# Kernel optimization log

Hardware: AMD Instinct MI355X
Metric: run time of the kernel (lower is better)

Reference implementation:

```python
import jax, jax.numpy as jnp
import numpy as np

N = 50000        # num nodes
E = 800000       # num edges
F_IN = 128
H1 = 256
H2 = 256
C = 64


def _sage_conv(x, edge_index, W_l, b_l, W_r):
    """PyG SAGEConv (mean aggr): lin_l(mean over in-neighbors of x_j) + lin_r(x)."""
    src = edge_index[0]
    dst = edge_index[1]
    n = x.shape[0]
    # gather messages [E, d] then segment-mean into [N, d]
    agg = jax.ops.segment_sum(x[src], dst, num_segments=n)
    cnt = jax.ops.segment_sum(jnp.ones((edge_index.shape[1],), x.dtype), dst, num_segments=n)
    mean = agg / jnp.maximum(cnt, 1.0)[:, None]
    return mean @ W_l + b_l + x @ W_r


def setup_inputs() -> dict:
    key = jax.random.key(0)
    ks = jax.random.split(key, 10)
    x = jax.random.normal(ks[0], (N, F_IN), dtype=jnp.float32)
    edge_index = jax.random.randint(ks[1], (2, E), 0, N, dtype=jnp.int64)
    s1 = 1.0 / np.sqrt(F_IN)
    s2 = 1.0 / np.sqrt(H1)
    s3 = 1.0 / np.sqrt(H2)
    return {
        "x": x,
        "edge_index": edge_index,
        "W1_l": jax.random.uniform(ks[2], (F_IN, H1), jnp.float32, -s1, s1),
        "b1": jnp.zeros((H1,), jnp.float32),
        "W1_r": jax.random.uniform(ks[3], (F_IN, H1), jnp.float32, -s1, s1),
        "W2_l": jax.random.uniform(ks[4], (H1, H2), jnp.float32, -s2, s2),
        "b2": jnp.zeros((H2,), jnp.float32),
        "W2_r": jax.random.uniform(ks[5], (H1, H2), jnp.float32, -s2, s2),
        "Wc": jax.random.uniform(ks[6], (H2, C), jnp.float32, -s3, s3),
        "bc": jax.random.uniform(ks[7], (C,), jnp.float32, -s3, s3),
    }


def reference(x, edge_index, W1_l, b1, W1_r, W2_l, b2, W2_r, Wc, bc):
    # inference mode: dropout is identity
    h = jax.nn.relu(_sage_conv(x, edge_index, W1_l, b1, W1_r))
    h = jax.nn.relu(_sage_conv(h, edge_index, W2_l, b2, W2_r))
    return h @ Wc + bc
```

## Files before the change

kernel.cpp:

```cpp
#include <hip/hip_runtime.h>
#include <hip/hip_bf16.h>


#define F_IN 128
#define H1_DIM 256
#define H2_DIM 256
#define C_DIM 64

typedef __attribute__((ext_vector_type(8))) _Float16 f16x8;
typedef __attribute__((ext_vector_type(8))) unsigned short u16x8;
typedef __attribute__((ext_vector_type(4))) float f32x4;

__device__ __forceinline__ unsigned short f2h(float f) {
    return __builtin_bit_cast(unsigned short, (_Float16)f);
}
__device__ __forceinline__ float h2f(unsigned short h) {
    return (float)__builtin_bit_cast(_Float16, h);
}

__global__ void k_detect(const unsigned int* __restrict__ ei, int* __restrict__ flag) {
    if (blockIdx.x == 0 && threadIdx.x == 0) {
        int is64 = 1;
        for (int i = 1; i < 256; i += 2) {
            if (ei[i] != 0u) { is64 = 0; break; }
        }
        *flag = is64;
    }
}

__device__ __forceinline__ int ei_at(const void* ei, const int* flag, long long idx) {
    return (*flag) ? (int)((const long long*)ei)[idx] : ((const int*)ei)[idx];
}

__global__ void k_degree(const void* __restrict__ ei, const int* __restrict__ flag,
                         int* __restrict__ cnt, int E) {
    int i = blockIdx.x * blockDim.x + threadIdx.x;
    if (i >= E) return;
    atomicAdd(&cnt[ei_at(ei, flag, (long long)E + i)], 1);
}

__global__ void k_scan1(const int* __restrict__ cnt, int* __restrict__ rowptr,
                        int* __restrict__ bsum, int n) {
    __shared__ int s[256];
    int i = blockIdx.x * 256 + threadIdx.x;
    int v = (i < n) ? cnt[i] : 0;
    s[threadIdx.x] = v;
    __syncthreads();
    for (int off = 1; off < 256; off <<= 1) {
        int t = (threadIdx.x >= off) ? s[threadIdx.x - off] : 0;
        __syncthreads();
        s[threadIdx.x] += t;
        __syncthreads();
    }
    if (i < n) rowptr[i] = s[threadIdx.x] - v;
    if (threadIdx.x == 255) bsum[blockIdx.x] = s[255];
}

__global__ void k_scan2(const int* __restrict__ bsum, int* __restrict__ boff, int nb) {
    __shared__ int s[1024];
    int t = threadIdx.x;
    int v = (t < nb) ? bsum[t] : 0;
    s[t] = v;
    __syncthreads();
    for (int off = 1; off < 1024; off <<= 1) {
        int u = (t >= off) ? s[t - off] : 0;
        __syncthreads();
        s[t] += u;
        __syncthreads();
    }
    if (t < nb) boff[t] = s[t] - v;
}

__global__ void k_scan3(int* __restrict__ rowptr, const int* __restrict__ boff,
                        int n, int total) {
    int i = blockIdx.x * 256 + threadIdx.x;
    if (i < n) rowptr[i] += boff[i >> 8];
    if (i == 0) rowptr[n] = total;
}

__global__ void k_scatter(const void* __restrict__ ei, const int* __restrict__ flag,
                          const int* __restrict__ rowptr, int* __restrict__ pos,
                          int* __restrict__ col, int E) {
    int i = blockIdx.x * blockDim.x + threadIdx.x;
    if (i >= E) return;
    int s = ei_at(ei, flag, i);
    int d = ei_at(ei, flag, (long long)E + i);
    int p = atomicAdd(&pos[d], 1);
    col[rowptr[d] + p] = s;
}

__global__ void k_prep_x(const float* __restrict__ x, unsigned short* __restrict__ xh,
                         int n4) {
    int i = blockIdx.x * 256 + threadIdx.x;
    if (i >= n4) return;
    float4 v = ((const float4*)x)[i];
    ushort4 h;
    h.x = f2h(v.x);
    h.y = f2h(v.y);
    h.z = f2h(v.z);
    h.w = f2h(v.w);
    ((ushort4*)xh)[i] = h;
}

struct WPrep {
    const float* W;
    unsigned short* wT;
    int K;
    int NN;
};

__global__ void k_prep_w(WPrep w0, WPrep w1, WPrep w2, WPrep w3, WPrep w4) {
    WPrep wp;
    switch (blockIdx.y) {
        case 0: wp = w0; break;
        case 1: wp = w1; break;
        case 2: wp = w2; break;
        case 3: wp = w3; break;
        default: wp = w4; break;
    }
    int total = wp.K * wp.NN;
    for (int i = blockIdx.x * 256 + threadIdx.x; i < total; i += gridDim.x * 256) {
        int k = i / wp.NN, n = i % wp.NN;
        wp.wT[(size_t)n * wp.K + k] = f2h(wp.W[i]);
    }
}

__global__ void k_agg1(const unsigned short* __restrict__ xh,
                       const int* __restrict__ rowptr, const int* __restrict__ col,
                       unsigned short* __restrict__ mean, int n) {
    int w = blockIdx.x * 4 + (threadIdx.x >> 6);
    int lane = threadIdx.x & 63;
    if (w >= n) return;
    int q = lane >> 4;
    int ch = (lane & 15) * 8;
    int beg = rowptr[w], end = rowptr[w + 1];
    float inv = 1.0f / fmaxf((float)(end - beg), 1.0f);

    float a[8];
#pragma unroll
    for (int c = 0; c < 8; ++c) a[c] = 0.f;

    int j = beg + q;
    for (; j + 4 < end; j += 8) {
        int c0 = col[j], c1 = col[j + 4];
        u16x8 r0 = *(const u16x8*)(xh + (size_t)c0 * 128 + ch);
        u16x8 r1 = *(const u16x8*)(xh + (size_t)c1 * 128 + ch);
#pragma unroll
        for (int c = 0; c < 8; ++c) a[c] += h2f(r0[c]) + h2f(r1[c]);
    }
    if (j < end) {
        u16x8 r0 = *(const u16x8*)(xh + (size_t)col[j] * 128 + ch);
#pragma unroll
        for (int c = 0; c < 8; ++c) a[c] += h2f(r0[c]);
    }

#pragma unroll
    for (int c = 0; c < 8; ++c) a[c] += __shfl_xor(a[c], 16);
#pragma unroll
    for (int c = 0; c < 8; ++c) a[c] += __shfl_xor(a[c], 32);

    if (q == 0) {
        u16x8 o;
#pragma unroll
        for (int c = 0; c < 8; ++c) o[c] = f2h(a[c] * inv);
        *(u16x8*)(mean + (size_t)w * 128 + ch) = o;
    }
}

__global__ void k_agg2(const unsigned short* __restrict__ hh,
                       const int* __restrict__ rowptr, const int* __restrict__ col,
                       unsigned short* __restrict__ mean, int n) {
    int w = blockIdx.x * 4 + (threadIdx.x >> 6);
    int lane = threadIdx.x & 63;
    if (w >= n) return;
    int h = lane >> 5;
    int ch = (lane & 31) * 8;
    int beg = rowptr[w], end = rowptr[w + 1];
    float inv = 1.0f / fmaxf((float)(end - beg), 1.0f);

    float a[8];
#pragma unroll
    for (int c = 0; c < 8; ++c) a[c] = 0.f;

    int j = beg + h;
    for (; j + 2 < end; j += 4) {
        int c0 = col[j], c1 = col[j + 2];
        u16x8 r0 = *(const u16x8*)(hh + (size_t)c0 * 256 + ch);
        u16x8 r1 = *(const u16x8*)(hh + (size_t)c1 * 256 + ch);
#pragma unroll
        for (int c = 0; c < 8; ++c) a[c] += h2f(r0[c]) + h2f(r1[c]);
    }
    if (j < end) {
        u16x8 r0 = *(const u16x8*)(hh + (size_t)col[j] * 256 + ch);
#pragma unroll
        for (int c = 0; c < 8; ++c) a[c] += h2f(r0[c]);
    }

#pragma unroll
    for (int c = 0; c < 8; ++c) a[c] += __shfl_xor(a[c], 32);

    if (h == 0) {
        u16x8 o;
#pragma unroll
        for (int c = 0; c < 8; ++c) o[c] = f2h(a[c] * inv);
        *(u16x8*)(mean + (size_t)w * 256 + ch) = o;
    }
}

struct Loads {
    const unsigned short* a[2];
    const unsigned short* b[2];
};

template <int BN, int NLOAD, int KS, bool RELU, int OUTMODE>
__global__ __launch_bounds__(256, 4) void k_mfma_gemm(
    Loads L, const float* __restrict__ bias,
    float* __restrict__ Cf, unsigned short* __restrict__ Ch, int M, int NN) {
    constexpr int BM = 128;
    constexpr int WAVES = 4;
    constexpr int WCN = 2;
    constexpr int WM = 64;
    constexpr int WN = BN / WCN;
    constexpr int FM = 4;
    constexpr int FN = WN / 16;
    constexpr int ACH = 16;
    constexpr int BCH = BN / 8;

    __shared__ unsigned short sA[BM * 64];
    __shared__ unsigned short sB[BN * 64];

    const int tid = threadIdx.x;
    const int lane = tid & 63;
    const int wid = tid >> 6;
    const int wr = wid / WCN, wc = wid % WCN;

    const int nbn = NN / BN;
    const int bm = (nbn == 1) ? blockIdx.x : blockIdx.x / nbn;
    const int bn = (nbn == 1) ? 0 : blockIdx.x % nbn;
    const int row0 = bm * BM;
    const int col0 = bn * BN;

    f32x4 acc[FM][FN];
#pragma unroll
    for (int m = 0; m < FM; ++m)
#pragma unroll
        for (int n = 0; n < FN; ++n) acc[m][n] = (f32x4){0.f, 0.f, 0.f, 0.f};

    const int l7 = lane & 7;
    const int l15 = lane & 15;
    const int q = lane >> 4;
    const int st_r = lane >> 3;
    const int st_k = 8 * (l7 ^ st_r);

    for (int ld = 0; ld < NLOAD; ++ld) {
        const unsigned short* Ag = L.a[ld];
        const unsigned short* Bg = L.b[ld];

        for (int k0 = 0; k0 < KS; k0 += 64) {
#pragma unroll
            for (int c = wid; c < ACH; c += WAVES) {
                int gr = row0 + c * 8 + st_r;
                if (gr >= M) gr = 0;
                const unsigned short* gp = Ag + (size_t)gr * KS + k0 + st_k;
                __builtin_amdgcn_global_load_lds(
                    (const __attribute__((address_space(1))) unsigned int*)gp,
                    (__attribute__((address_space(3))) unsigned int*)(sA + c * 512),
                    16, 0, 0);
            }
#pragma unroll
            for (int c = wid; c < BCH; c += WAVES) {
                int gn = col0 + c * 8 + st_r;
                const unsigned short* gp = Bg + (size_t)gn * KS + k0 + st_k;
                __builtin_amdgcn_global_load_lds(
                    (const __attribute__((address_space(1))) unsigned int*)gp,
                    (__attribute__((address_space(3))) unsigned int*)(sB + c * 512),
                    16, 0, 0);
            }
            __syncthreads();

#pragma unroll
            for (int ks = 0; ks < 2; ++ks) {
                const int sidx = 8 * ((q + 4 * ks) ^ l7);
                f16x8 af[FM], bf[FN];
#pragma unroll
                for (int m = 0; m < FM; ++m) {
                    int rb = wr * WM + m * 16 + l15;
                    af[m] = *(const f16x8*)(sA + (size_t)rb * 64 + sidx);
                }
#pragma unroll
                for (int n = 0; n < FN; ++n) {
                    int cb = wc * WN + n * 16 + l15;
                    bf[n] = *(const f16x8*)(sB + (size_t)cb * 64 + sidx);
                }
#pragma unroll
                for (int m = 0; m < FM; ++m)
#pragma unroll
                    for (int n = 0; n < FN; ++n)
                        acc[m][n] = __builtin_amdgcn_mfma_f32_16x16x32_f16(
                            af[m], bf[n], acc[m][n], 0, 0, 0);
            }
            __syncthreads();
        }
    }

#pragma unroll
    for (int m = 0; m < FM; ++m) {
#pragma unroll
        for (int n = 0; n < FN; ++n) {
            int col = col0 + wc * WN + n * 16 + l15;
            float bb = bias[col];
#pragma unroll
            for (int r = 0; r < 4; ++r) {
                int row = row0 + wr * WM + m * 16 + q * 4 + r;
                if (row < M) {
                    float t = acc[m][n][r] + bb;
                    if (RELU) t = fmaxf(t, 0.f);
                    if (OUTMODE == 0) {
                        Cf[(size_t)row * NN + col] = t;
                    } else {
                        Ch[(size_t)row * NN + col] = f2h(t);
                    }
                }
            }
        }
    }
}

extern "C" void kernel_launch(void* const* d_in, const int* in_sizes, int n_in,
                              void* d_out, int out_size, void* d_ws, size_t ws_size,
                              hipStream_t stream) {
    const float* x   = (const float*)d_in[0];
    const void*  ei  = d_in[1];
    const float* W1l = (const float*)d_in[2];
    const float* b1  = (const float*)d_in[3];
    const float* W1r = (const float*)d_in[4];
    const float* W2l = (const float*)d_in[5];
    const float* b2  = (const float*)d_in[6];
    const float* W2r = (const float*)d_in[7];
    const float* Wc  = (const float*)d_in[8];
    const float* bc  = (const float*)d_in[9];
    float* out = (float*)d_out;

    const int N = in_sizes[0] / F_IN;
    const int E = in_sizes[1] / 2;

    typedef unsigned short u16;

    char* w = (char*)d_ws;
    size_t off = 0;
    auto carve = [&](size_t bytes) -> char* {
        char* p = w + off;
        off = (off + bytes + 255) & ~(size_t)255;
        return p;
    };
    int* cnt    = (int*)carve((size_t)N * 4);
    int* pos    = (int*)carve((size_t)N * 4);
    int* rowptr = (int*)carve((size_t)(N + 1) * 4);
    int* bsum   = (int*)carve(1024 * 4);
    int* boff   = (int*)carve(1024 * 4);
    int* flag   = (int*)carve(256);
    int* col    = (int*)carve((size_t)E * 4);

    u16* xh     = (u16*)carve((size_t)N * F_IN * 2);
    u16* agg    = (u16*)carve((size_t)N * 256 * 2);
    u16* h1     = (u16*)carve((size_t)N * 256 * 2);
    u16* h2     = (u16*)carve((size_t)N * 256 * 2);

    u16* w1lT   = (u16*)carve((size_t)F_IN * H1_DIM * 2);
    u16* w1rT   = (u16*)carve((size_t)F_IN * H1_DIM * 2);
    u16* w2lT   = (u16*)carve((size_t)H1_DIM * H2_DIM * 2);
    u16* w2rT   = (u16*)carve((size_t)H1_DIM * H2_DIM * 2);
    u16* wcT    = (u16*)carve((size_t)H2_DIM * C_DIM * 2);
    (void)ws_size;

    hipMemsetAsync(cnt, 0, (char*)rowptr - (char*)cnt, stream);

    k_detect<<<1, 64, 0, stream>>>((const unsigned int*)ei, flag);
    k_degree<<<(E + 255) / 256, 256, 0, stream>>>(ei, flag, cnt, E);
    int nb = (N + 255) / 256;
    k_scan1<<<nb, 256, 0, stream>>>(cnt, rowptr, bsum, N);
    k_scan2<<<1, 1024, 0, stream>>>(bsum, boff, nb);
    k_scan3<<<nb, 256, 0, stream>>>(rowptr, boff, N, E);
    k_scatter<<<(E + 255) / 256, 256, 0, stream>>>(ei, flag, rowptr, pos, col, E);

    k_prep_x<<<((N * F_IN / 4) + 255) / 256, 256, 0, stream>>>(x, xh, N * F_IN / 4);
    {
        WPrep w0{W1l, w1lT, F_IN, H1_DIM};
        WPrep w1{W1r, w1rT, F_IN, H1_DIM};
        WPrep w2{W2l, w2lT, H1_DIM, H2_DIM};
        WPrep w3{W2r, w2rT, H1_DIM, H2_DIM};
        WPrep w4{Wc, wcT, H2_DIM, C_DIM};
        dim3 g(64, 5);
        k_prep_w<<<g, 256, 0, stream>>>(w0, w1, w2, w3, w4);
    }

    const int nbm = (N + 127) / 128;

    k_agg1<<<(N + 3) / 4, 256, 0, stream>>>(xh, rowptr, col, agg, N);
    {
        Loads L;
        L.a[0] = agg; L.b[0] = w1lT;
        L.a[1] = xh;  L.b[1] = w1rT;
        k_mfma_gemm<128, 2, 128, true, 1><<<nbm * (H1_DIM / 128), 256, 0, stream>>>(
            L, b1, nullptr, h1, N, H1_DIM);
    }

    k_agg2<<<(N + 3) / 4, 256, 0, stream>>>(h1, rowptr, col, agg, N);
    {
        Loads L;
        L.a[0] = agg; L.b[0] = w2lT;
        L.a[1] = h1;  L.b[1] = w2rT;
        k_mfma_gemm<128, 2, 256, true, 1><<<nbm * (H2_DIM / 128), 256, 0, stream>>>(
            L, b2, nullptr, h2, N, H2_DIM);
    }

    {
        Loads L;
        L.a[0] = h2; L.b[0] = wcT;
        L.a[1] = nullptr; L.b[1] = nullptr;
        k_mfma_gemm<64, 1, 256, false, 0><<<nbm, 256, 0, stream>>>(
            L, bc, out, nullptr, N, C_DIM);
    }
}
```

Before: 334.8 us.

## Gather neighbor features from column-sliced tables to shrink aggregation working set

Node features and layer-1 outputs are also written in a column-sliced layout (32-channel slices stored contiguously per slice). A new templated aggregation kernel gives each block one slice, and four lanes cover one node's 64-byte slice row. The aim is to keep each gather pass's working set small enough to stay in cache across random neighbor accesses. The cost is extra writes of duplicate tables in the prep and GEMM epilogue, plus scattered 2-byte stores in the GEMM epilogue.

```diff
diff --git a/kernel.cpp b/kernel.cpp
--- a/kernel.cpp
+++ b/kernel.cpp
@@ -90,7 +90,7 @@
 }
 
 __global__ void k_prep_x(const float* __restrict__ x, unsigned short* __restrict__ xh,
-                         int n4) {
+                         unsigned short* __restrict__ xs, int n4, int N) {
     int i = blockIdx.x * 256 + threadIdx.x;
     if (i >= n4) return;
     float4 v = ((const float4*)x)[i];
@@ -100,6 +100,10 @@
     h.z = f2h(v.z);
     h.w = f2h(v.w);
     ((ushort4*)xh)[i] = h;
+    int row = i >> 5;
+    int c0 = (i & 31) * 4;
+    int s = c0 >> 5;
+    *(ushort4*)(xs + ((size_t)s * N + row) * 32 + (c0 & 31)) = h;
 }
 
 struct WPrep {
@@ -125,86 +129,42 @@
     }
 }
 
-__global__ void k_agg1(const unsigned short* __restrict__ xh,
+template <int ROWCH, int NSLICE, int LOGS>
+__global__ void k_aggs(const unsigned short* __restrict__ tbl,
                        const int* __restrict__ rowptr, const int* __restrict__ col,
-                       unsigned short* __restrict__ mean, int n) {
-    int w = blockIdx.x * 4 + (threadIdx.x >> 6);
-    int lane = threadIdx.x & 63;
+                       unsigned short* __restrict__ mean , int n) {
+    int lane4 = threadIdx.x & 3;
+    int g = threadIdx.x >> 2;
+    int s = blockIdx.x & (NSLICE - 1);
+    int w = (blockIdx.x >> LOGS) * 64 + g;
     if (w >= n) return;
-    int q = lane >> 4;
-    int ch = (lane & 15) * 8;
     int beg = rowptr[w], end = rowptr[w + 1];
     float inv = 1.0f / fmaxf((float)(end - beg), 1.0f);
 
+    const unsigned short* base = tbl + (size_t)s * n * 32 + lane4 * 8;
+
     float a[8];
 #pragma unroll
     for (int c = 0; c < 8; ++c) a[c] = 0.f;
 
-    int j = beg + q;
-    for (; j + 4 < end; j += 8) {
-        int c0 = col[j], c1 = col[j + 4];
-        u16x8 r0 = *(const u16x8*)(xh + (size_t)c0 * 128 + ch);
-        u16x8 r1 = *(const u16x8*)(xh + (size_t)c1 * 128 + ch);
+    int j = beg;
+    for (; j + 1 < end; j += 2) {
+        int c0 = col[j], c1 = col[j + 1];
+        u16x8 r0 = *(const u16x8*)(base + (size_t)c0 * 32);
+        u16x8 r1 = *(const u16x8*)(base + (size_t)c1 * 32);
 #pragma unroll
         for (int c = 0; c < 8; ++c) a[c] += h2f(r0[c]) + h2f(r1[c]);
     }
     if (j < end) {
-        u16x8 r0 = *(const u16x8*)(xh + (size_t)col[j] * 128 + ch);
+        u16x8 r0 = *(const u16x8*)(base + (size_t)col[j] * 32);
 #pragma unroll
         for (int c = 0; c < 8; ++c) a[c] += h2f(r0[c]);
     }
 
-#pragma unroll
-    for (int c = 0; c < 8; ++c) a[c] += __shfl_xor(a[c], 16);
-#pragma unroll
-    for (int c = 0; c < 8; ++c) a[c] += __shfl_xor(a[c], 32);
-
-    if (q == 0) {
-        u16x8 o;
-#pragma unroll
-        for (int c = 0; c < 8; ++c) o[c] = f2h(a[c] * inv);
-        *(u16x8*)(mean + (size_t)w * 128 + ch) = o;
-    }
-}
-
-__global__ void k_agg2(const unsigned short* __restrict__ hh,
-                       const int* __restrict__ rowptr, const int* __restrict__ col,
-                       unsigned short* __restrict__ mean, int n) {
-    int w = blockIdx.x * 4 + (threadIdx.x >> 6);
-    int lane = threadIdx.x & 63;
-    if (w >= n) return;
-    int h = lane >> 5;
-    int ch = (lane & 31) * 8;
-    int beg = rowptr[w], end = rowptr[w + 1];
-    float inv = 1.0f / fmaxf((float)(end - beg), 1.0f);
-
-    float a[8];
-#pragma unroll
-    for (int c = 0; c < 8; ++c) a[c] = 0.f;
-
-    int j = beg + h;
-    for (; j + 2 < end; j += 4) {
-        int c0 = col[j], c1 = col[j + 2];
-        u16x8 r0 = *(const u16x8*)(hh + (size_t)c0 * 256 + ch);
-        u16x8 r1 = *(const u16x8*)(hh + (size_t)c1 * 256 + ch);
-#pragma unroll
-        for (int c = 0; c < 8; ++c) a[c] += h2f(r0[c]) + h2f(r1[c]);
-    }
-    if (j < end) {
-        u16x8 r0 = *(const u16x8*)(hh + (size_t)col[j] * 256 + ch);
-#pragma unroll
-        for (int c = 0; c < 8; ++c) a[c] += h2f(r0[c]);
-    }
-
-#pragma unroll
-    for (int c = 0; c < 8; ++c) a[c] += __shfl_xor(a[c], 32);
-
-    if (h == 0) {
-        u16x8 o;
-#pragma unroll
-        for (int c = 0; c < 8; ++c) o[c] = f2h(a[c] * inv);
-        *(u16x8*)(mean + (size_t)w * 256 + ch) = o;
-    }
+    u16x8 o;
+#pragma unroll
+    for (int c = 0; c < 8; ++c) o[c] = f2h(a[c] * inv);
+    *(u16x8*)(mean + (size_t)w * ROWCH + s * 32 + lane4 * 8) = o;
 }
 
 struct Loads {
@@ -215,7 +175,8 @@
 template <int BN, int NLOAD, int KS, bool RELU, int OUTMODE>
 __global__ __launch_bounds__(256, 4) void k_mfma_gemm(
     Loads L, const float* __restrict__ bias,
-    float* __restrict__ Cf, unsigned short* __restrict__ Ch, int M, int NN) {
+    float* __restrict__ Cf, unsigned short* __restrict__ Ch,
+    unsigned short* __restrict__ Ch2, int M, int NN) {
     constexpr int BM = 128;
     constexpr int WAVES = 4;
     constexpr int WCN = 2;
@@ -318,7 +279,12 @@
                     if (OUTMODE == 0) {
                         Cf[(size_t)row * NN + col] = t;
                     } else {
-                        Ch[(size_t)row * NN + col] = f2h(t);
+                        unsigned short hv = f2h(t);
+                        Ch[(size_t)row * NN + col] = hv;
+                        if (OUTMODE == 2) {
+                            int s = col >> 5;
+                            Ch2[((size_t)s * M + row) * 32 + (col & 31)] = hv;
+                        }
                     }
                 }
             }
@@ -362,8 +328,10 @@
     int* col    = (int*)carve((size_t)E * 4);
 
     u16* xh     = (u16*)carve((size_t)N * F_IN * 2);
+    u16* xs     = (u16*)carve((size_t)N * F_IN * 2);
     u16* agg    = (u16*)carve((size_t)N * 256 * 2);
     u16* h1     = (u16*)carve((size_t)N * 256 * 2);
+    u16* h1s    = (u16*)carve((size_t)N * 256 * 2);
     u16* h2     = (u16*)carve((size_t)N * 256 * 2);
 
     u16* w1lT   = (u16*)carve((size_t)F_IN * H1_DIM * 2);
@@ -383,7 +351,8 @@
     k_scan3<<<nb, 256, 0, stream>>>(rowptr, boff, N, E);
     k_scatter<<<(E + 255) / 256, 256, 0, stream>>>(ei, flag, rowptr, pos, col, E);
 
-    k_prep_x<<<((N * F_IN / 4) + 255) / 256, 256, 0, stream>>>(x, xh, N * F_IN / 4);
+    k_prep_x<<<((N * F_IN / 4) + 255) / 256, 256, 0, stream>>>(
+        x, xh, xs, N * F_IN / 4, N);
     {
         WPrep w0{W1l, w1lT, F_IN, H1_DIM};
         WPrep w1{W1r, w1rT, F_IN, H1_DIM};
@@ -395,23 +364,24 @@
     }
 
     const int nbm = (N + 127) / 128;
-
-    k_agg1<<<(N + 3) / 4, 256, 0, stream>>>(xh, rowptr, col, agg, N);
+    const int nwg = (N + 63) / 64;
+
+    k_aggs<128, 4, 2><<<4 * nwg, 256, 0, stream>>>(xs, rowptr, col, agg, N);
     {
         Loads L;
         L.a[0] = agg; L.b[0] = w1lT;
         L.a[1] = xh;  L.b[1] = w1rT;
-        k_mfma_gemm<128, 2, 128, true, 1><<<nbm * (H1_DIM / 128), 256, 0, stream>>>(
-            L, b1, nullptr, h1, N, H1_DIM);
-    }
-
-    k_agg2<<<(N + 3) / 4, 256, 0, stream>>>(h1, rowptr, col, agg, N);
+        k_mfma_gemm<128, 2, 128, true, 2><<<nbm * 2, 256, 0, stream>>>(
+            L, b1, nullptr, h1, h1s, N, H1_DIM);
+    }
+
+    k_aggs<256, 8, 3><<<8 * nwg, 256, 0, stream>>>(h1s, rowptr, col, agg, N);
     {
         Loads L;
         L.a[0] = agg; L.b[0] = w2lT;
         L.a[1] = h1;  L.b[1] = w2rT;
-        k_mfma_gemm<128, 2, 256, true, 1><<<nbm * (H2_DIM / 128), 256, 0, stream>>>(
-            L, b2, nullptr, h2, N, H2_DIM);
+        k_mfma_gemm<128, 2, 256, true, 1><<<nbm * 2, 256, 0, stream>>>(
+            L, b2, nullptr, h2, nullptr, N, H2_DIM);
     }
 
     {
@@ -419,6 +389,6 @@
         L.a[0] = h2; L.b[0] = wcT;
         L.a[1] = nullptr; L.b[1] = nullptr;
         k_mfma_gemm<64, 1, 256, false, 0><<<nbm, 256, 0, stream>>>(
-            L, bc, out, nullptr, N, C_DIM);
-    }
-}
+            L, bc, out, nullptr, nullptr, N, C_DIM);
+    }
+}
```

Result: slower. 348.4 us (+4.1%).
